# Kernel optimization log

Hardware: AMD Instinct MI355X
Metric: run time of the kernel (lower is better)

## Reference

```python
import jax, jax.numpy as jnp
import numpy as np

B, SQ, SKV = 32, 200, 200
D, HEADS, L, V, FF = 1024, 16, 6, 32000, 2048
HD = D // HEADS
EPS = 1e-9


def _pe(seq_len, d):
    # sinusoidal positional encoding, matching PositionalEncoding
    pos = jnp.arange(seq_len, dtype=jnp.float32)[:, None]
    div = jnp.power(10000.0, jnp.arange(0, d, 2, dtype=jnp.float32) / d)
    ang = pos / div
    pe = jnp.zeros((seq_len, d), dtype=jnp.float32)
    pe = pe.at[:, 0::2].set(jnp.sin(ang))
    pe = pe.at[:, 1::2].set(jnp.cos(ang))
    return pe


def _ln(x, g, b):
    m = x.mean(-1, keepdims=True)
    v = ((x - m) ** 2).mean(-1, keepdims=True)  # unbiased=False
    return (x - m) / jnp.sqrt(v + EPS) * g + b


def _mha(xq, xk, xv, Wq, bq, Wk, bk, Wv, bv, Wo, mask):
    b, sq, _ = xq.shape
    sk = xk.shape[1]
    q = (xq @ Wq + bq).reshape(b, sq, HEADS, HD).transpose(0, 2, 1, 3)
    k = (xk @ Wk + bk).reshape(b, sk, HEADS, HD).transpose(0, 2, 1, 3)
    v = (xv @ Wv + bv).reshape(b, sk, HEADS, HD).transpose(0, 2, 1, 3)
    scores = jnp.einsum('bhqd,bhkd->bhqk', q, k) / jnp.float32(np.sqrt(HD))
    if mask is not None:
        scores = jnp.where(mask, -jnp.inf, scores)
    attn = jax.nn.softmax(scores, axis=-1)
    o = jnp.einsum('bhqk,bhkd->bhqd', attn, v).transpose(0, 2, 1, 3).reshape(b, sq, D)
    return o @ Wo


def setup_inputs() -> dict:
    key0 = jax.random.key(0)
    ks = list(jax.random.split(key0, 24))
    s = 0.02
    inp = {}
    # token ids in [1, V): avoid pad id 0 so no fully-masked softmax row (NaN)
    inp['query'] = jax.random.randint(ks[0], (B, SQ), 1, V)
    inp['key'] = jax.random.normal(ks[1], (B, SKV, D), jnp.float32)
    inp['value'] = jax.random.normal(ks[2], (B, SKV, D), jnp.float32)
    inp['emb'] = jax.random.normal(ks[3], (V, D), jnp.float32) * s
    for i, nm in enumerate(['ln1_g', 'ln2_g', 'ln3_g']):
        inp[nm] = jnp.ones((L, D), jnp.float32)
    for nm in ['ln1_b', 'ln2_b', 'ln3_b']:
        inp[nm] = jnp.zeros((L, D), jnp.float32)
    names = ['Wq_s', 'Wk_s', 'Wv_s', 'Wo_s', 'Wq_c', 'Wk_c', 'Wv_c', 'Wo_c']
    for i, nm in enumerate(names):
        inp[nm] = jax.random.normal(ks[4 + i], (L, D, D), jnp.float32) * s
    for nm in ['bq_s', 'bk_s', 'bv_s', 'bq_c', 'bk_c', 'bv_c']:
        inp[nm] = jnp.zeros((L, D), jnp.float32)
    inp['W1'] = jax.random.normal(ks[12], (L, D, FF), jnp.float32) * s
    inp['bf1'] = jnp.zeros((L, FF), jnp.float32)
    inp['W2'] = jax.random.normal(ks[13], (L, FF, D), jnp.float32) * s
    inp['bf2'] = jnp.zeros((L, D), jnp.float32)
    inp['lnf_g'] = jnp.ones((D,), jnp.float32)
    inp['lnf_b'] = jnp.zeros((D,), jnp.float32)
    return inp


def reference(query, key, value, emb, ln1_g, ln1_b, ln2_g, ln2_b, ln3_g, ln3_b,
              Wq_s, bq_s, Wk_s, bk_s, Wv_s, bv_s, Wo_s,
              Wq_c, bq_c, Wk_c, bk_c, Wv_c, bv_c, Wo_c,
              W1, bf1, W2, bf2, lnf_g, lnf_b):
    x = emb[query] + _pe(SQ, D)[None]  # dropout is identity at eval
    causal = jnp.triu(jnp.ones((SQ, SQ), dtype=bool), 1)[None, None]
    pad = (query == 0)[:, None, None, :]
    self_mask = causal | pad  # [B,1,SQ,SQ]
    o = x
    for l in range(L):
        qn = _ln(o, ln1_g[l], ln1_b[l])
        sa = _mha(qn, qn, qn, Wq_s[l], bq_s[l], Wk_s[l], bk_s[l], Wv_s[l], bv_s[l], Wo_s[l], self_mask)
        o1 = o + sa
        an = _ln(o1, ln2_g[l], ln2_b[l])
        ca = _mha(an, key, value, Wq_c[l], bq_c[l], Wk_c[l], bk_c[l], Wv_c[l], bv_c[l], Wo_c[l], None)
        o2 = o1 + ca
        cn = _ln(o2, ln3_g[l], ln3_b[l])
        ff = jax.nn.relu(cn @ W1[l] + bf1[l]) @ W2[l] + bf2[l]
        o = o2 + ff
    return _ln(o, lnf_g, lnf_b)
```

## Files before the change

kernel.cpp:

```cpp
#include <hip/hip_runtime.h>
#include <math.h>

#define BB  32
#define SQl 200
#define SKV 200
#define DD  1024
#define NH  16
#define HDm 64
#define NL  6
#define FFD 2048

typedef __attribute__((ext_vector_type(8))) short  short8v;
typedef __attribute__((ext_vector_type(4))) float  floatx4;

#define SBAR()  asm volatile("s_barrier" ::: "memory")
#define VMCNT6() asm volatile("s_waitcnt vmcnt(6)" ::: "memory")
#define VMCNT0() asm volatile("s_waitcnt vmcnt(0)" ::: "memory")

__device__ __forceinline__ ushort f2bf(float x) {
  uint u = __builtin_bit_cast(uint, x);
  u = (u + 0x7FFFu + ((u >> 16) & 1u)) >> 16;
  return (ushort)u;
}

__device__ __forceinline__ void gll16(const void* g, void* l) {
  __builtin_amdgcn_global_load_lds((const __attribute__((address_space(1))) void*)g,
                                   (__attribute__((address_space(3))) void*)l,
                                   16, 0, 0);
}

__global__ __launch_bounds__(256) void embed_pe_kernel(const int* __restrict__ qids,
                                                       const float* __restrict__ emb,
                                                       float* __restrict__ x) {
  int idx = blockIdx.x * 256 + threadIdx.x;
  int d   = idx & (DD - 1);
  int row = idx >> 10;
  int s   = row % SQl;
  int tok = qids[row];
  float expo = (float)(d & ~1) * (1.0f / (float)DD);
  float dv   = powf(10000.0f, expo);
  float ang  = (float)s / dv;
  float pe   = (d & 1) ? cosf(ang) : sinf(ang);
  x[idx] = emb[(size_t)tok * DD + d] + pe;
}

__global__ __launch_bounds__(256) void cvt_bf16_kernel(const float* __restrict__ in,
                                                       ushort* __restrict__ out, int n8) {
  int idx = blockIdx.x * 256 + threadIdx.x;
  if (idx >= n8) return;
  const floatx4 va = ((const floatx4*)in)[idx * 2];
  const floatx4 vb = ((const floatx4*)in)[idx * 2 + 1];
  short8v o;
  o[0] = (short)f2bf(va.x); o[1] = (short)f2bf(va.y);
  o[2] = (short)f2bf(va.z); o[3] = (short)f2bf(va.w);
  o[4] = (short)f2bf(vb.x); o[5] = (short)f2bf(vb.y);
  o[6] = (short)f2bf(vb.z); o[7] = (short)f2bf(vb.w);
  ((short8v*)out)[idx] = o;
}

struct P8 { const float* p[8]; };
__global__ __launch_bounds__(256) void transpose48_kernel(P8 srcs, ushort* __restrict__ dst) {
  __shared__ float t[32][33];
  const size_t MEL = (size_t)DD * DD;
  const int z = blockIdx.z;
  const int arr = z / 6, l = z - arr * 6;
  const size_t base[8] = {0, MEL, 2*MEL, 18*MEL, 24*MEL, 30*MEL, 36*MEL, 42*MEL};
  const size_t lstr[8] = {3*MEL, 3*MEL, 3*MEL, MEL, MEL, MEL, MEL, MEL};
  const float* __restrict__ W = srcs.p[arr] + (size_t)l * MEL;
  ushort* __restrict__ WT = dst + base[arr] + (size_t)l * lstr[arr];
  const int n0 = blockIdx.x * 32, k0 = blockIdx.y * 32;
  const int tx = threadIdx.x & 31, ty = threadIdx.x >> 5;
#pragma unroll
  for (int i = 0; i < 4; ++i)
    t[ty + i * 8][tx] = W[(size_t)(k0 + ty + i * 8) * DD + n0 + tx];
  __syncthreads();
#pragma unroll
  for (int i = 0; i < 4; ++i)
    WT[(size_t)(n0 + ty + i * 8) * DD + k0 + tx] = f2bf(t[tx][ty + i * 8]);
}

__global__ __launch_bounds__(256) void transposeW_kernel(const float* __restrict__ src,
                                                         ushort* __restrict__ dst,
                                                         int K, int N) {
  __shared__ float t[32][33];
  const int z = blockIdx.z;
  const float* __restrict__ W = src + (size_t)z * K * N;
  ushort* __restrict__ WT = dst + (size_t)z * K * N;
  const int n0 = blockIdx.x * 32, k0 = blockIdx.y * 32;
  const int tx = threadIdx.x & 31, ty = threadIdx.x >> 5;
#pragma unroll
  for (int i = 0; i < 4; ++i)
    t[ty + i * 8][tx] = W[(size_t)(k0 + ty + i * 8) * N + n0 + tx];
  __syncthreads();
#pragma unroll
  for (int i = 0; i < 4; ++i)
    WT[(size_t)(n0 + ty + i * 8) * K + k0 + tx] = f2bf(t[tx][ty + i * 8]);
}

template <int OBF16>
__global__ __launch_bounds__(256) void ln4_kernel(const float* __restrict__ in,
                                                  const float* __restrict__ gam,
                                                  const float* __restrict__ bet,
                                                  float* __restrict__ outf,
                                                  ushort* __restrict__ outb) {
  const int wid  = threadIdx.x >> 6;
  const int lane = threadIdx.x & 63;
  const int row  = blockIdx.x * 4 + wid;
  const float* ip = in + (size_t)row * DD;

  float4 x[4];
  float s = 0.f, sq = 0.f;
#pragma unroll
  for (int i = 0; i < 4; ++i) {
    x[i] = *(const float4*)&ip[i * 256 + lane * 4];
    s  += x[i].x + x[i].y + x[i].z + x[i].w;
    sq += x[i].x * x[i].x + x[i].y * x[i].y + x[i].z * x[i].z + x[i].w * x[i].w;
  }
#pragma unroll
  for (int msk = 1; msk < 64; msk <<= 1) {
    s  += __shfl_xor(s,  msk, 64);
    sq += __shfl_xor(sq, msk, 64);
  }
  const float m   = s * (1.0f / (float)DD);
  const float var = sq * (1.0f / (float)DD) - m * m;
  const float inv = rsqrtf(var + 1e-9f);

#pragma unroll
  for (int i = 0; i < 4; ++i) {
    const int c = i * 256 + lane * 4;
    const float4 g4 = *(const float4*)&gam[c];
    const float4 b4 = *(const float4*)&bet[c];
    float o0 = (x[i].x - m) * inv * g4.x + b4.x;
    float o1 = (x[i].y - m) * inv * g4.y + b4.y;
    float o2 = (x[i].z - m) * inv * g4.z + b4.z;
    float o3 = (x[i].w - m) * inv * g4.w + b4.w;
    if (OBF16) {
      uint2 pk;
      pk.x = (uint)f2bf(o0) | ((uint)f2bf(o1) << 16);
      pk.y = (uint)f2bf(o2) | ((uint)f2bf(o3) << 16);
      *(uint2*)&outb[(size_t)row * DD + c] = pk;
    } else {
      float4 ov; ov.x = o0; ov.y = o1; ov.z = o2; ov.w = o3;
      *(float4*)&outf[(size_t)row * DD + c] = ov;
    }
  }
}

struct BiasP { const float* p[6]; };
template <int RELU, int ACC, int OBF16>
__global__ __launch_bounds__(512) void gemm8_mfma(const ushort* __restrict__ A,
                                                  const ushort* __restrict__ BT,
                                                  BiasP bias,
                                                  float* __restrict__ C,
                                                  ushort* __restrict__ Cb,
                                                  int M, int N, int K, int ldc) {
  __shared__ short8v As[3 * 2048];
  __shared__ short8v Bs[3 * 1024];
  const int tid  = threadIdx.x;
  const int w    = tid >> 6;
  const int lane = tid & 63;
  const int bm = blockIdx.y * 256;
  const int bn = blockIdx.x * 128;
  const int wm = (w >> 1) * 64;
  const int wn = (w & 1) * 64;
  const int lq = lane & 15;
  const int lg = lane >> 4;

  const ushort* aS[4];
  const ushort* bS[2];
#pragma unroll
  for (int i = 0; i < 4; ++i) {
    const int s   = w * 64 + i * 512 + lane;
    const int row = s >> 3;
    const int kg  = (s & 7) ^ (row & 7);
    aS[i] = A + (size_t)(bm + row) * K + kg * 8;
  }
#pragma unroll
  for (int i = 0; i < 2; ++i) {
    const int s   = w * 64 + i * 512 + lane;
    const int row = s >> 3;
    const int kg  = (s & 7) ^ (row & 7);
    bS[i] = BT + (size_t)(bn + row) * K + kg * 8;
  }

  int aIdx[4], bIdx[4];
#pragma unroll
  for (int i = 0; i < 4; ++i) {
    const int mr = wm + i * 16 + lq;
    aIdx[i] = mr * 8 + (lg ^ (mr & 7));
    const int nr = wn + i * 16 + lq;
    bIdx[i] = nr * 8 + (lg ^ (nr & 7));
  }

  floatx4 acc[4][4];
  const floatx4 fz = {0.f, 0.f, 0.f, 0.f};
#pragma unroll
  for (int mi = 0; mi < 4; ++mi)
#pragma unroll
    for (int ni = 0; ni < 4; ++ni) acc[mi][ni] = fz;

  const int nt = K >> 6;

#pragma unroll
  for (int b = 0; b < 2; ++b) {
    const int koff = b * 64;
    gll16(aS[0] + koff, &As[b * 2048 + w * 64 + 0 * 512]);
    gll16(aS[1] + koff, &As[b * 2048 + w * 64 + 1 * 512]);
    gll16(aS[2] + koff, &As[b * 2048 + w * 64 + 2 * 512]);
    gll16(aS[3] + koff, &As[b * 2048 + w * 64 + 3 * 512]);
    gll16(bS[0] + koff, &Bs[b * 1024 + w * 64 + 0 * 512]);
    gll16(bS[1] + koff, &Bs[b * 1024 + w * 64 + 1 * 512]);
  }
  VMCNT6();
  SBAR();

  int cur = 0;
  for (int t = 0; t < nt; ++t) {
    int b2 = cur + 2; if (b2 >= 3) b2 -= 3;
    const int koff2 = (t + 2) * 64;
    const bool pf = (t + 2) < nt;
    const int cbA = cur * 2048, cbB = cur * 1024;
    short8v* dA = &As[b2 * 2048 + w * 64];
    short8v* dB = &Bs[b2 * 1024 + w * 64];

    short8v af[4], bf_[4];
#pragma unroll
    for (int i = 0; i < 4; ++i) { af[i] = As[cbA + aIdx[i]]; bf_[i] = Bs[cbB + bIdx[i]]; }
    if (pf) {
      gll16(aS[0] + koff2, dA + 0 * 512);
      gll16(aS[1] + koff2, dA + 1 * 512);
      gll16(bS[0] + koff2, dB + 0 * 512);
    }
    SBAR();
    __builtin_amdgcn_s_setprio(1);
#pragma unroll
    for (int mi = 0; mi < 4; ++mi)
#pragma unroll
      for (int ni = 0; ni < 4; ++ni)
        acc[mi][ni] = __builtin_amdgcn_mfma_f32_16x16x32_bf16(af[mi], bf_[ni], acc[mi][ni], 0, 0, 0);
    __builtin_amdgcn_s_setprio(0);
    SBAR();

#pragma unroll
    for (int i = 0; i < 4; ++i) { af[i] = As[cbA + (aIdx[i] ^ 4)]; bf_[i] = Bs[cbB + (bIdx[i] ^ 4)]; }
    if (pf) {
      gll16(aS[2] + koff2, dA + 2 * 512);
      gll16(aS[3] + koff2, dA + 3 * 512);
      gll16(bS[1] + koff2, dB + 1 * 512);
    }
    SBAR();
    __builtin_amdgcn_s_setprio(1);
#pragma unroll
    for (int mi = 0; mi < 4; ++mi)
#pragma unroll
      for (int ni = 0; ni < 4; ++ni)
        acc[mi][ni] = __builtin_amdgcn_mfma_f32_16x16x32_bf16(af[mi], bf_[ni], acc[mi][ni], 0, 0, 0);
    __builtin_amdgcn_s_setprio(0);

    if (pf) { VMCNT6(); } else { VMCNT0(); }
    SBAR();
    cur = cur + 1; if (cur >= 3) cur -= 3;
  }

#pragma unroll
  for (int mi = 0; mi < 4; ++mi) {
    const int row = bm + wm + mi * 16 + lg * 4;
#pragma unroll
    for (int ni = 0; ni < 4; ++ni) {
      const int col = bn + wn + ni * 16 + lq;
      const float* bp = bias.p[col >> 10];
      const float bvv = bp ? bp[col & (DD - 1)] : 0.f;
#pragma unroll
      for (int r = 0; r < 4; ++r) {
        float val = acc[mi][ni][r] + bvv;
        if (ACC)  val += C[(size_t)(row + r) * ldc + col];
        if (RELU) val = fmaxf(val, 0.f);
        if (OBF16) Cb[(size_t)(row + r) * ldc + col] = f2bf(val);
        else       C [(size_t)(row + r) * ldc + col] = val;
      }
    }
  }
}

static inline void launch_g(const ushort* A, const ushort* BT, BiasP bias,
                            float* C, ushort* Cb, int M, int N, int K, int ldc,
                            int mode, hipStream_t s) {
  dim3 grid(N / 128, M / 256), blk(512);
  if (mode == 1)      gemm8_mfma<0, 1, 0><<<grid, blk, 0, s>>>(A, BT, bias, C, Cb, M, N, K, ldc);
  else if (mode == 2) gemm8_mfma<1, 0, 1><<<grid, blk, 0, s>>>(A, BT, bias, C, Cb, M, N, K, ldc);
  else                gemm8_mfma<0, 0, 1><<<grid, blk, 0, s>>>(A, BT, bias, C, Cb, M, N, K, ldc);
}

template <int CAUSAL>
__global__ __launch_bounds__(256, 2) void attn_mfma_kernel(const ushort* __restrict__ q, int qs,
                                                           const ushort* __restrict__ k, int ks,
                                                           const ushort* __restrict__ v, int vs,
                                                           const int* __restrict__ qids,
                                                           ushort* __restrict__ out) {
  __shared__ short8v Kl[208 * 8];
  __shared__ ushort  Vt[64 * 256];
  __shared__ short8v Pl[1024];
  __shared__ float   padf[224];

  const int bh   = blockIdx.x;
  const int h    = bh & (NH - 1);
  const int b    = bh >> 4;
  const int tid  = threadIdx.x;
  const int w    = tid >> 6;
  const int lane = tid & 63;
  const int lq   = lane & 15;
  const int lg   = lane >> 4;

  if (tid < 208) {
    const int kp = tid;
    if (kp < SKV) {
      const short8v* src = (const short8v*)(k + ((size_t)(b * SKV + kp)) * ks + h * HDm);
#pragma unroll
      for (int s = 0; s < 8; ++s) Kl[kp * 8 + (s ^ (kp & 7))] = src[s];
    } else {
      const short8v z = {0, 0, 0, 0, 0, 0, 0, 0};
#pragma unroll
      for (int s = 0; s < 8; ++s) Kl[kp * 8 + s] = z;
    }
  }
  if (tid < 224) {
    const int kp = tid;
    float pf = 1.f;
    if (kp < SKV) {
      pf = CAUSAL ? ((qids[b * SQl + kp] == 0) ? 1.f : 0.f) : 0.f;
      const short8v* src = (const short8v*)(v + ((size_t)(b * SKV + kp)) * vs + h * HDm);
      const int s3 = kp >> 3, k7 = kp & 7;
#pragma unroll
      for (int li = 0; li < 8; ++li) {
        const short8v vv = src[li];
#pragma unroll
        for (int e = 0; e < 8; ++e)
          Vt[(li * 8 + e) * 256 + ((s3 ^ e) * 8) + k7] = (ushort)vv[e];
      }
    } else {
      const int s3 = kp >> 3, k7 = kp & 7;
#pragma unroll
      for (int li = 0; li < 8; ++li)
#pragma unroll
        for (int e = 0; e < 8; ++e)
          Vt[(li * 8 + e) * 256 + ((s3 ^ e) * 8) + k7] = 0;
    }
    padf[kp] = pf;
  }
  __syncthreads();

  short8v qf[4][2];
#pragma unroll
  for (int i = 0; i < 4; ++i) {
    const int mt = i * 4 + w;
    if (mt > 12) continue;
    int qrow = mt * 16 + lq;
    if (qrow > SQl - 1) qrow = SQl - 1;
    const ushort* qp = q + ((size_t)(b * SQl + qrow)) * qs + h * HDm + lg * 8;
    qf[i][0] = *(const short8v*)qp;
    qf[i][1] = *(const short8v*)(qp + 32);
  }

  float rmax[4][4];
#pragma unroll
  for (int i = 0; i < 4; ++i)
#pragma unroll
    for (int r = 0; r < 4; ++r) rmax[i][r] = -3e38f;

  for (int kt = 0; kt < 13; ++kt) {
    const int kp = kt * 16 + lq;
    const short8v bk0 = Kl[kp * 8 + (lg ^ (kp & 7))];
    const short8v bk1 = Kl[kp * 8 + ((4 + lg) ^ (kp & 7))];
    const float pmask = padf[kp];
#pragma unroll
    for (int i = 0; i < 4; ++i) {
      const int mt = i * 4 + w;
      if (mt > 12) continue;
      floatx4 S = {0.f, 0.f, 0.f, 0.f};
      S = __builtin_amdgcn_mfma_f32_16x16x32_bf16(qf[i][0], bk0, S, 0, 0, 0);
      S = __builtin_amdgcn_mfma_f32_16x16x32_bf16(qf[i][1], bk1, S, 0, 0, 0);
#pragma unroll
      for (int r = 0; r < 4; ++r) {
        const int qrow = mt * 16 + lg * 4 + r;
        bool masked = (pmask != 0.f);
        if (CAUSAL) masked = masked || (kp > qrow);
        const float s = masked ? -3e38f : S[r] * 0.125f;
        rmax[i][r] = fmaxf(rmax[i][r], s);
      }
    }
  }
#pragma unroll
  for (int msk = 1; msk < 16; msk <<= 1)
#pragma unroll
    for (int i = 0; i < 4; ++i)
#pragma unroll
      for (int r = 0; r < 4; ++r)
        rmax[i][r] = fmaxf(rmax[i][r], __shfl_xor(rmax[i][r], msk, 64));

  float rsum[4][4];
  floatx4 Of[4][4];
  const floatx4 fz = {0.f, 0.f, 0.f, 0.f};
#pragma unroll
  for (int i = 0; i < 4; ++i)
#pragma unroll
    for (int r = 0; r < 4; ++r) { rsum[i][r] = 0.f; Of[i][r] = fz; }

  for (int kc = 0; kc < 7; ++kc) {
#pragma unroll
    for (int t = 0; t < 2; ++t) {
      const int kt = kc * 2 + t;
      const int kp = kt * 16 + lq;
      short8v bk0, bk1;
      float pmask = 1.f;
      if (kt < 13) {
        bk0 = Kl[kp * 8 + (lg ^ (kp & 7))];
        bk1 = Kl[kp * 8 + ((4 + lg) ^ (kp & 7))];
        pmask = padf[kp];
      }
#pragma unroll
      for (int i = 0; i < 4; ++i) {
        const int mt = i * 4 + w;
        if (mt > 12) continue;
        floatx4 S = {0.f, 0.f, 0.f, 0.f};
        if (kt < 13) {
          S = __builtin_amdgcn_mfma_f32_16x16x32_bf16(qf[i][0], bk0, S, 0, 0, 0);
          S = __builtin_amdgcn_mfma_f32_16x16x32_bf16(qf[i][1], bk1, S, 0, 0, 0);
        }
#pragma unroll
        for (int r = 0; r < 4; ++r) {
          const int qrow = mt * 16 + lg * 4 + r;
          bool masked = (kt >= 13) || (pmask != 0.f);
          if (CAUSAL) masked = masked || (kp > qrow);
          const float p = masked ? 0.f : __expf(S[r] * 0.125f - rmax[i][r]);
          rsum[i][r] += p;
          const int qrl  = lg * 4 + r;
          const int kpl  = t * 16 + lq;
          const int slot = (kpl >> 3) ^ ((qrl >> 2) & 3);
          ((ushort*)Pl)[(w * 4 + i) * 512 + qrl * 32 + slot * 8 + (kpl & 7)] = f2bf(p);
        }
      }
    }
    short8v vb[4];
#pragma unroll
    for (int dt = 0; dt < 4; ++dt) {
      const int d  = dt * 16 + lq;
      const int sk = kc * 4 + lg;
      vb[dt] = ((const short8v*)Vt)[d * 32 + (sk ^ (d & 7))];
    }
#pragma unroll
    for (int i = 0; i < 4; ++i) {
      const int mt = i * 4 + w;
      if (mt > 12) continue;
      const short8v pa = Pl[(w * 4 + i) * 64 + lq * 4 + (lg ^ ((lq >> 2) & 3))];
#pragma unroll
      for (int dt = 0; dt < 4; ++dt)
        Of[i][dt] = __builtin_amdgcn_mfma_f32_16x16x32_bf16(pa, vb[dt], Of[i][dt], 0, 0, 0);
    }
  }

#pragma unroll
  for (int msk = 1; msk < 16; msk <<= 1)
#pragma unroll
    for (int i = 0; i < 4; ++i)
#pragma unroll
      for (int r = 0; r < 4; ++r)
        rsum[i][r] += __shfl_xor(rsum[i][r], msk, 64);

#pragma unroll
  for (int i = 0; i < 4; ++i) {
    const int mt = i * 4 + w;
    if (mt > 12) continue;
#pragma unroll
    for (int r = 0; r < 4; ++r) {
      const int qrow = mt * 16 + lg * 4 + r;
      if (qrow >= SQl) continue;
      const float linv = 1.0f / rsum[i][r];
      ushort* op = out + ((size_t)(b * SQl + qrow)) * DD + h * HDm;
#pragma unroll
      for (int dt = 0; dt < 4; ++dt)
        op[dt * 16 + lq] = f2bf(Of[i][dt][r] * linv);
    }
  }
}

extern "C" void kernel_launch(void* const* d_in, const int* in_sizes, int n_in,
                              void* d_out, int out_size, void* d_ws, size_t ws_size,
                              hipStream_t stream) {
  (void)in_sizes; (void)n_in; (void)out_size; (void)ws_size;

  const int*   qids  = (const int*)  d_in[0];
  const float* key   = (const float*)d_in[1];
  const float* value = (const float*)d_in[2];
  const float* emb   = (const float*)d_in[3];
  const float* ln1_g = (const float*)d_in[4];
  const float* ln2_g = (const float*)d_in[5];
  const float* ln3_g = (const float*)d_in[6];
  const float* ln1_b = (const float*)d_in[7];
  const float* ln2_b = (const float*)d_in[8];
  const float* ln3_b = (const float*)d_in[9];
  const float* Wq_s  = (const float*)d_in[10];
  const float* Wk_s  = (const float*)d_in[11];
  const float* Wv_s  = (const float*)d_in[12];
  const float* Wo_s  = (const float*)d_in[13];
  const float* Wq_c  = (const float*)d_in[14];
  const float* Wk_c  = (const float*)d_in[15];
  const float* Wv_c  = (const float*)d_in[16];
  const float* Wo_c  = (const float*)d_in[17];
  const float* bq_s  = (const float*)d_in[18];
  const float* bk_s  = (const float*)d_in[19];
  const float* bv_s  = (const float*)d_in[20];
  const float* bq_c  = (const float*)d_in[21];
  const float* bk_c  = (const float*)d_in[22];
  const float* bv_c  = (const float*)d_in[23];
  const float* W1    = (const float*)d_in[24];
  const float* bf1   = (const float*)d_in[25];
  const float* W2    = (const float*)d_in[26];
  const float* bf2   = (const float*)d_in[27];
  const float* lnf_g = (const float*)d_in[28];
  const float* lnf_b = (const float*)d_in[29];

  const size_t NTOK = (size_t)BB * SQl * DD;
  const size_t MEL  = (size_t)DD * DD;
  char* w = (char*)d_ws;
  float*  o    = (float*)w;  w += NTOK * 4;
  ushort* t0b  = (ushort*)w; w += NTOK * 2;
  ushort* qkv  = (ushort*)w; w += (size_t)BB * SQl * 3 * DD * 2;
  ushort* kc   = (ushort*)w; w += (size_t)BB * SQl * 6 * DD * 2;
  ushort* vc   = (ushort*)w; w += (size_t)BB * SQl * 6 * DD * 2;
  ushort* kb   = (ushort*)w; w += NTOK * 2;
  ushort* vb   = (ushort*)w; w += NTOK * 2;
  ushort* fbb  = (ushort*)w; w += (size_t)BB * SQl * FFD * 2;
  ushort* wt   = (ushort*)w; w += 48 * MEL * 2;
  ushort* wt1  = (ushort*)w; w += (size_t)NL * DD * FFD * 2;
  ushort* wt2  = (ushort*)w; w += (size_t)NL * FFD * DD * 2;

  const int M = BB * SQl;
  const BiasP nob = {{nullptr, nullptr, nullptr, nullptr, nullptr, nullptr}};

  embed_pe_kernel<<<(int)(NTOK / 256), 256, 0, stream>>>(qids, emb, o);
  cvt_bf16_kernel<<<(int)(NTOK / 8 + 255) / 256, 256, 0, stream>>>(key,   kb, (int)(NTOK / 8));
  cvt_bf16_kernel<<<(int)(NTOK / 8 + 255) / 256, 256, 0, stream>>>(value, vb, (int)(NTOK / 8));

  P8 p8 = {{Wq_s, Wk_s, Wv_s, Wo_s, Wq_c, Wk_c, Wv_c, Wo_c}};
  transpose48_kernel<<<dim3(32, 32, 48), 256, 0, stream>>>(p8, wt);
  transposeW_kernel<<<dim3(FFD / 32, DD / 32, NL), 256, 0, stream>>>(W1, wt1, DD, FFD);
  transposeW_kernel<<<dim3(DD / 32, FFD / 32, NL), 256, 0, stream>>>(W2, wt2, FFD, DD);

  ushort* wtQKV = wt;
  ushort* wtOs  = wt + 18 * MEL;
  ushort* wtQc  = wt + 24 * MEL;
  ushort* wtKc  = wt + 30 * MEL;
  ushort* wtVc  = wt + 36 * MEL;
  ushort* wtOc  = wt + 42 * MEL;

  {
    BiasP bk6, bv6;
#pragma unroll
    for (int l = 0; l < NL; ++l) { bk6.p[l] = bk_c + l * DD; bv6.p[l] = bv_c + l * DD; }
    launch_g(kb, wtKc, bk6, nullptr, kc, M, 6 * DD, DD, 6 * DD, 3, stream);
    launch_g(vb, wtVc, bv6, nullptr, vc, M, 6 * DD, DD, 6 * DD, 3, stream);
  }

  for (int l = 0; l < NL; ++l) {
    ln4_kernel<1><<<M / 4, 256, 0, stream>>>(o, ln1_g + l * DD, ln1_b + l * DD, nullptr, t0b);
    BiasP bqkv = {{bq_s + l * DD, bk_s + l * DD, bv_s + l * DD, nullptr, nullptr, nullptr}};
    launch_g(t0b, wtQKV + l * 3 * MEL, bqkv, nullptr, qkv, M, 3 * DD, DD, 3 * DD, 3, stream);
    attn_mfma_kernel<1><<<BB * NH, 256, 0, stream>>>(qkv, 3 * DD, qkv + DD, 3 * DD,
                                                     qkv + 2 * DD, 3 * DD, qids, t0b);
    launch_g(t0b, wtOs + l * MEL, nob, o, nullptr, M, DD, DD, DD, 1, stream);

    ln4_kernel<1><<<M / 4, 256, 0, stream>>>(o, ln2_g + l * DD, ln2_b + l * DD, nullptr, t0b);
    BiasP bqc = {{bq_c + l * DD, nullptr, nullptr, nullptr, nullptr, nullptr}};
    launch_g(t0b, wtQc + l * MEL, bqc, nullptr, qkv, M, DD, DD, 3 * DD, 3, stream);
    attn_mfma_kernel<0><<<BB * NH, 256, 0, stream>>>(qkv, 3 * DD, kc + l * DD, 6 * DD,
                                                     vc + l * DD, 6 * DD, nullptr, t0b);
    launch_g(t0b, wtOc + l * MEL, nob, o, nullptr, M, DD, DD, DD, 1, stream);

    ln4_kernel<1><<<M / 4, 256, 0, stream>>>(o, ln3_g + l * DD, ln3_b + l * DD, nullptr, t0b);
    BiasP bf1p = {{bf1 + l * FFD, bf1 + l * FFD + DD, nullptr, nullptr, nullptr, nullptr}};
    launch_g(t0b, wt1 + (size_t)l * DD * FFD, bf1p, nullptr, fbb, M, FFD, DD, FFD, 2, stream);
    BiasP bf2p = {{bf2 + l * DD, nullptr, nullptr, nullptr, nullptr, nullptr}};
    launch_g(fbb, wt2 + (size_t)l * FFD * DD, bf2p, o, nullptr, M, DD, FFD, DD, 1, stream);
  }

  ln4_kernel<0><<<M / 4, 256, 0, stream>>>(o, lnf_g, lnf_b, (float*)d_out, nullptr);
}
```

Measured before the change: 2.633 ms.

## Add 256x256-tile double-buffered GEMM for wide outputs and simplify pipeline

Adds a new GEMM kernel with 256x256 output tiles, 8 waves each computing 128x64, and double-buffered LDS. It is used when N >= 2048 (fused QKV, FF1 and the like), raising arithmetic intensity per loaded byte. The existing 256x128 kernel now issues all prefetch loads at the top of each iteration and drops the intermediate barriers. The barrier macro also switches to the compiler builtin. Risks are higher register pressure from 32 accumulators per wave, occupancy limits from launch_bounds(512,2), fewer blocks for wave quantization, and a full vmcnt(0) wait each iteration in the new kernel.

Result: slower. 2.932 ms (+11.4%).

```diff
diff --git a/kernel.cpp b/kernel.cpp
--- a/kernel.cpp
+++ b/kernel.cpp
@@ -13,7 +13,7 @@
 typedef __attribute__((ext_vector_type(8))) short  short8v;
 typedef __attribute__((ext_vector_type(4))) float  floatx4;
 
-#define SBAR()  asm volatile("s_barrier" ::: "memory")
+#define SBAR()   __builtin_amdgcn_s_barrier()
 #define VMCNT6() asm volatile("s_waitcnt vmcnt(6)" ::: "memory")
 #define VMCNT0() asm volatile("s_waitcnt vmcnt(0)" ::: "memory")
 
@@ -147,6 +147,116 @@
 }
 
 struct BiasP { const float* p[6]; };
+
+template <int RELU, int ACC, int OBF16>
+__global__ __launch_bounds__(512, 2) void gemm256_mfma(const ushort* __restrict__ A,
+                                                       const ushort* __restrict__ BT,
+                                                       BiasP bias,
+                                                       float* __restrict__ C,
+                                                       ushort* __restrict__ Cb,
+                                                       int M, int N, int K, int ldc) {
+  __shared__ short8v As[2 * 2048];
+  __shared__ short8v Bs[2 * 2048];
+  const int tid  = threadIdx.x;
+  const int w    = tid >> 6;
+  const int lane = tid & 63;
+  const int bm = blockIdx.y * 256;
+  const int bn = blockIdx.x * 256;
+  const int wm = (w >> 2) * 128;
+  const int wn = (w & 3) * 64;
+  const int lq = lane & 15;
+  const int lg = lane >> 4;
+
+  const ushort* aS[4];
+  const ushort* bS[4];
+#pragma unroll
+  for (int i = 0; i < 4; ++i) {
+    const int s   = i * 512 + tid;
+    const int row = s >> 3;
+    const int kg  = (s & 7) ^ (row & 7);
+    aS[i] = A  + (size_t)(bm + row) * K + kg * 8;
+    bS[i] = BT + (size_t)(bn + row) * K + kg * 8;
+  }
+
+  int aIdx[8], bIdx[4];
+#pragma unroll
+  for (int i = 0; i < 8; ++i) {
+    const int mr = wm + i * 16 + lq;
+    aIdx[i] = mr * 8 + (lg ^ (mr & 7));
+  }
+#pragma unroll
+  for (int i = 0; i < 4; ++i) {
+    const int nr = wn + i * 16 + lq;
+    bIdx[i] = nr * 8 + (lg ^ (nr & 7));
+  }
+
+  floatx4 acc[8][4];
+  const floatx4 fz = {0.f, 0.f, 0.f, 0.f};
+#pragma unroll
+  for (int mi = 0; mi < 8; ++mi)
+#pragma unroll
+    for (int ni = 0; ni < 4; ++ni) acc[mi][ni] = fz;
+
+  const int nt = K >> 6;
+
+#pragma unroll
+  for (int i = 0; i < 4; ++i) gll16(aS[i], &As[i * 512 + w * 64]);
+#pragma unroll
+  for (int i = 0; i < 4; ++i) gll16(bS[i], &Bs[i * 512 + w * 64]);
+  VMCNT0();
+  SBAR();
+
+  int cur = 0;
+  for (int t = 0; t < nt; ++t) {
+    if (t + 1 < nt) {
+      const int ko = (t + 1) * 64;
+      const int db = (cur ^ 1) * 2048;
+#pragma unroll
+      for (int i = 0; i < 4; ++i) gll16(aS[i] + ko, &As[db + i * 512 + w * 64]);
+#pragma unroll
+      for (int i = 0; i < 4; ++i) gll16(bS[i] + ko, &Bs[db + i * 512 + w * 64]);
+    }
+    const int cb = cur * 2048;
+#pragma unroll
+    for (int kk = 0; kk < 2; ++kk) {
+      short8v af[8], bf_[4];
+#pragma unroll
+      for (int i = 0; i < 8; ++i) af[i]  = As[cb + (aIdx[i] ^ (kk * 4))];
+#pragma unroll
+      for (int i = 0; i < 4; ++i) bf_[i] = Bs[cb + (bIdx[i] ^ (kk * 4))];
+      __builtin_amdgcn_s_setprio(1);
+#pragma unroll
+      for (int mi = 0; mi < 8; ++mi)
+#pragma unroll
+        for (int ni = 0; ni < 4; ++ni)
+          acc[mi][ni] = __builtin_amdgcn_mfma_f32_16x16x32_bf16(af[mi], bf_[ni], acc[mi][ni], 0, 0, 0);
+      __builtin_amdgcn_s_setprio(0);
+    }
+    VMCNT0();
+    SBAR();
+    cur ^= 1;
+  }
+
+#pragma unroll
+  for (int mi = 0; mi < 8; ++mi) {
+    const int row = bm + wm + mi * 16 + lg * 4;
+#pragma unroll
+    for (int ni = 0; ni < 4; ++ni) {
+      const int col = bn + wn + ni * 16 + lq;
+      const float* bp = bias.p[col >> 10];
+      const float bvv = bp ? bp[col & (DD - 1)] : 0.f;
+#pragma unroll
+      for (int r = 0; r < 4; ++r) {
+        float val = acc[mi][ni][r] + bvv;
+        if (ACC)  val += C[(size_t)(row + r) * ldc + col];
+        if (RELU) val = fmaxf(val, 0.f);
+        if (OBF16) Cb[(size_t)(row + r) * ldc + col] = f2bf(val);
+        else       C [(size_t)(row + r) * ldc + col] = val;
+      }
+    }
+  }
+}
+
 template <int RELU, int ACC, int OBF16>
 __global__ __launch_bounds__(512) void gemm8_mfma(const ushort* __restrict__ A,
                                                   const ushort* __restrict__ BT,
@@ -217,46 +327,35 @@
   int cur = 0;
   for (int t = 0; t < nt; ++t) {
     int b2 = cur + 2; if (b2 >= 3) b2 -= 3;
-    const int koff2 = (t + 2) * 64;
     const bool pf = (t + 2) < nt;
+    if (pf) {
+      const int ko = (t + 2) * 64;
+      short8v* dA = &As[b2 * 2048 + w * 64];
+      short8v* dB = &Bs[b2 * 1024 + w * 64];
+      gll16(aS[0] + ko, dA + 0 * 512);
+      gll16(aS[1] + ko, dA + 1 * 512);
+      gll16(aS[2] + ko, dA + 2 * 512);
+      gll16(aS[3] + ko, dA + 3 * 512);
+      gll16(bS[0] + ko, dB + 0 * 512);
+      gll16(bS[1] + ko, dB + 1 * 512);
+    }
     const int cbA = cur * 2048, cbB = cur * 1024;
-    short8v* dA = &As[b2 * 2048 + w * 64];
-    short8v* dB = &Bs[b2 * 1024 + w * 64];
-
-    short8v af[4], bf_[4];
-#pragma unroll
-    for (int i = 0; i < 4; ++i) { af[i] = As[cbA + aIdx[i]]; bf_[i] = Bs[cbB + bIdx[i]]; }
-    if (pf) {
-      gll16(aS[0] + koff2, dA + 0 * 512);
-      gll16(aS[1] + koff2, dA + 1 * 512);
-      gll16(bS[0] + koff2, dB + 0 * 512);
-    }
-    SBAR();
-    __builtin_amdgcn_s_setprio(1);
-#pragma unroll
-    for (int mi = 0; mi < 4; ++mi)
-#pragma unroll
-      for (int ni = 0; ni < 4; ++ni)
-        acc[mi][ni] = __builtin_amdgcn_mfma_f32_16x16x32_bf16(af[mi], bf_[ni], acc[mi][ni], 0, 0, 0);
-    __builtin_amdgcn_s_setprio(0);
-    SBAR();
-
-#pragma unroll
-    for (int i = 0; i < 4; ++i) { af[i] = As[cbA + (aIdx[i] ^ 4)]; bf_[i] = Bs[cbB + (bIdx[i] ^ 4)]; }
-    if (pf) {
-      gll16(aS[2] + koff2, dA + 2 * 512);
-      gll16(aS[3] + koff2, dA + 3 * 512);
-      gll16(bS[1] + koff2, dB + 1 * 512);
-    }
-    SBAR();
-    __builtin_amdgcn_s_setprio(1);
-#pragma unroll
-    for (int mi = 0; mi < 4; ++mi)
-#pragma unroll
-      for (int ni = 0; ni < 4; ++ni)
-        acc[mi][ni] = __builtin_amdgcn_mfma_f32_16x16x32_bf16(af[mi], bf_[ni], acc[mi][ni], 0, 0, 0);
-    __builtin_amdgcn_s_setprio(0);
-
+#pragma unroll
+    for (int kk = 0; kk < 2; ++kk) {
+      short8v af[4], bf_[4];
+#pragma unroll
+      for (int i = 0; i < 4; ++i) {
+        af[i]  = As[cbA + (aIdx[i] ^ (kk * 4))];
+        bf_[i] = Bs[cbB + (bIdx[i] ^ (kk * 4))];
+      }
+      __builtin_amdgcn_s_setprio(1);
+#pragma unroll
+      for (int mi = 0; mi < 4; ++mi)
+#pragma unroll
+        for (int ni = 0; ni < 4; ++ni)
+          acc[mi][ni] = __builtin_amdgcn_mfma_f32_16x16x32_bf16(af[mi], bf_[ni], acc[mi][ni], 0, 0, 0);
+      __builtin_amdgcn_s_setprio(0);
+    }
     if (pf) { VMCNT6(); } else { VMCNT0(); }
     SBAR();
     cur = cur + 1; if (cur >= 3) cur -= 3;
@@ -285,10 +384,17 @@
 static inline void launch_g(const ushort* A, const ushort* BT, BiasP bias,
                             float* C, ushort* Cb, int M, int N, int K, int ldc,
                             int mode, hipStream_t s) {
-  dim3 grid(N / 128, M / 256), blk(512);
-  if (mode == 1)      gemm8_mfma<0, 1, 0><<<grid, blk, 0, s>>>(A, BT, bias, C, Cb, M, N, K, ldc);
-  else if (mode == 2) gemm8_mfma<1, 0, 1><<<grid, blk, 0, s>>>(A, BT, bias, C, Cb, M, N, K, ldc);
-  else                gemm8_mfma<0, 0, 1><<<grid, blk, 0, s>>>(A, BT, bias, C, Cb, M, N, K, ldc);
+  if (N >= 2048) {
+    dim3 grid(N / 256, M / 256), blk(512);
+    if (mode == 1)      gemm256_mfma<0, 1, 0><<<grid, blk, 0, s>>>(A, BT, bias, C, Cb, M, N, K, ldc);
+    else if (mode == 2) gemm256_mfma<1, 0, 1><<<grid, blk, 0, s>>>(A, BT, bias, C, Cb, M, N, K, ldc);
+    else                gemm256_mfma<0, 0, 1><<<grid, blk, 0, s>>>(A, BT, bias, C, Cb, M, N, K, ldc);
+  } else {
+    dim3 grid(N / 128, M / 256), blk(512);
+    if (mode == 1)      gemm8_mfma<0, 1, 0><<<grid, blk, 0, s>>>(A, BT, bias, C, Cb, M, N, K, ldc);
+    else if (mode == 2) gemm8_mfma<1, 0, 1><<<grid, blk, 0, s>>>(A, BT, bias, C, Cb, M, N, K, ldc);
+    else                gemm8_mfma<0, 0, 1><<<grid, blk, 0, s>>>(A, BT, bias, C, Cb, M, N, K, ldc);
+  }
 }
 
 template <int CAUSAL>
```
